# Kernel optimization log

Hardware: AMD Instinct MI355X
Metric: run time of the kernel (lower is better)

Reference implementation:

```python
import jax, jax.numpy as jnp
import numpy as np

CH = 16
HID = 128
UPDATE_RATE = 0.25

def _perception_kernel():
    identity = jnp.array([[0.,0.,0.],[0.,1.,0.],[0.,0.,0.]], jnp.float32)
    sobel_x = jnp.array([[-1.,0.,1.],[-2.,0.,2.],[-1.,0.,1.]], jnp.float32)
    sobel_y = sobel_x.T
    laplacian = jnp.array([[1.,1.,1.],[1.,-8.,1.],[1.,1.,1.]], jnp.float32)
    k = jnp.stack([identity, sobel_x, sobel_y, laplacian])[:, None, :, :]  # [4,1,3,3]
    return jnp.tile(k, (CH, 1, 1, 1))  # [4*CH,1,3,3], OIHW depthwise

def setup_inputs() -> dict:
    key = jax.random.key(0)
    ks = jax.random.split(key, 10)
    B, H, W = 32, 256, 256
    x = jax.random.normal(ks[0], (B, CH, H, W), jnp.float32)
    # 1x1 conv weights: stored as [out,in]; biases [out]
    def lin(k, o, i, scale):
        return jax.random.normal(k, (o, i), jnp.float32) * scale
    w1 = lin(ks[1], HID, CH*4, 1.0/np.sqrt(CH*4)); b1 = jnp.zeros((HID,), jnp.float32)
    w2 = lin(ks[2], HID, HID, 1.0/np.sqrt(HID)); b2 = jnp.zeros((HID,), jnp.float32)
    w3 = lin(ks[3], HID, HID, 1.0/np.sqrt(HID)); b3 = jnp.zeros((HID,), jnp.float32)
    # last layer initialized to zero in original; use small random so gradients flow meaningfully
    w4 = lin(ks[4], CH, HID, 0.01)
    # precomputed random update mask (torch.rand < rate), constant w.r.t. grads
    update_mask = (jax.random.uniform(ks[5], (B, 1, H, W)) < UPDATE_RATE).astype(jnp.float32)
    return {"x": x, "w1": w1, "b1": b1, "w2": w2, "b2": b2, "w3": w3, "b3": b3, "w4": w4, "update_mask": update_mask, "steps": 1}

def _alive_mask(x, threshold=0.01):
    alpha = x[:, :2, :, :]
    pool = jax.lax.reduce_window(alpha, -jnp.inf, jax.lax.max,
                                 (1, 1, 3, 3), (1, 1, 1, 1),
                                 ((0, 0), (0, 0), (1, 1), (1, 1)))
    s = jnp.sum(jnp.abs(pool), axis=1, keepdims=True)  # [B,1,H,W]
    return (s > threshold).astype(x.dtype)

def _step(x, params, update_mask, kernel):
    w1, b1, w2, b2, w3, b3, w4 = params
    pre_alive = _alive_mask(x)
    # depthwise 3x3 perception conv: [B,CH,H,W] -> [B,4*CH,H,W]
    y = jax.lax.conv_general_dilated(x, kernel, (1, 1), ((1, 1), (1, 1)),
                                     dimension_numbers=('NCHW', 'OIHW', 'NCHW'),
                                     feature_group_count=CH)
    lrelu = lambda z: jax.nn.leaky_relu(z, 0.01)
    h = lrelu(jnp.einsum('oc,bchw->bohw', w1, y) + b1[None, :, None, None])
    h = lrelu(jnp.einsum('oc,bchw->bohw', w2, h) + b2[None, :, None, None])
    h = lrelu(jnp.einsum('oc,bchw->bohw', w3, h) + b3[None, :, None, None])
    dy = jnp.einsum('oc,bchw->bohw', w4, h)
    x = x + dy * update_mask
    post_alive = _alive_mask(x)
    return x * (pre_alive * post_alive)

def reference(x, w1, b1, w2, b2, w3, b3, w4, update_mask, steps):
    kernel = _perception_kernel()
    params = (w1, b1, w2, b2, w3, b3, w4)
    for _ in range(steps):
        x = _step(x, params, update_mask, kernel)
    return x
```

## Files before the change

### kernel.cpp

```cpp
#include <hip/hip_runtime.h>

typedef _Float16 f16;
typedef f16 f16x2 __attribute__((ext_vector_type(2)));
typedef f16 f16x8 __attribute__((ext_vector_type(8)));
typedef __fp16 h2v __attribute__((ext_vector_type(2)));
typedef float f32x4 __attribute__((ext_vector_type(4)));
typedef float f32x16 __attribute__((ext_vector_type(16)));
typedef unsigned int uint;
typedef unsigned short ushort;
typedef unsigned long long ull;

#define NCH 16
#define NB 32
#define NH 256
#define NW 256
#define HW 65536
#define CHW 1048576

#define BIAS_BYTE 90112
#define WS_BYTES 91648
#define LIST_OFF WS_BYTES
#define CTR_OFF (WS_BYTES + 12*256*2)
#define LDS_TOTAL (CTR_OFF + 16)

__global__ void prep_k(const float* __restrict__ w1, const float* __restrict__ w2,
                       const float* __restrict__ w3, const float* __restrict__ w4,
                       const float* __restrict__ b1, const float* __restrict__ b2,
                       const float* __restrict__ b3, float* __restrict__ wsf) {
  f16* wf = (f16*)wsf;
  int id = blockIdx.x * 256 + threadIdx.x;
  if (id < 8192) {
    int j = id & 7, l = (id >> 3) & 63, mt = (id >> 9) & 3, kt = id >> 11;
    int o = mt * 32 + (l & 31), c = kt * 16 + (l >> 5) * 8 + j;
    wf[id] = (f16)w1[o * 64 + c];
  } else if (id < 24576) {
    int t = id - 8192;
    int j = t & 7, l = (t >> 3) & 63, mt = (t >> 9) & 3, kt = t >> 11;
    int o = mt * 32 + (l & 31), c = kt * 16 + (l >> 5) * 8 + j;
    wf[8192 + t] = (f16)w2[o * 128 + c];
  } else if (id < 40960) {
    int t = id - 24576;
    int j = t & 7, l = (t >> 3) & 63, mt = (t >> 9) & 3, kt = t >> 11;
    int o = mt * 32 + (l & 31), c = kt * 16 + (l >> 5) * 8 + j;
    wf[24576 + t] = (f16)w3[o * 128 + c];
  } else if (id < 45056) {
    int t = id - 40960;
    int j = t & 7, l = (t >> 3) & 63, kt = t >> 9;
    int m = l & 31, hh = l >> 5;
    int c = kt * 16 + hh * 8 + j;
    wf[40960 + t] = (m < 16) ? (f16)w4[m * 128 + c] : (f16)0.f;
  } else if (id < 45440) {
    int t = id - 45056;
    int r = t & 15, hh = (t >> 4) & 1, mt = (t >> 5) & 3, ly = t >> 7;
    const float* bb = (ly == 0) ? b1 : (ly == 1) ? b2 : b3;
    ((float*)((unsigned char*)wsf + BIAS_BYTE))[t] =
        bb[mt * 32 + (r & 3) + 8 * (r >> 2) + 4 * hh];
  }
}

__global__ __launch_bounds__(256)
void copy_k(const float4* __restrict__ x4, float4* __restrict__ xn4) {
  const size_t total = (size_t)NB * CHW / 4;
  for (size_t i = (size_t)blockIdx.x * 256 + threadIdx.x; i < total; i += (size_t)2048 * 256)
    xn4[i] = x4[i];
}

__device__ __forceinline__ void pl32swap(uint& a, uint& b) {
  asm volatile("v_permlane32_swap_b32 %0, %1" : "+v"(a), "+v"(b));
}

__device__ __forceinline__ f16x8 mk8(uint a, uint b, uint c, uint d) {
  union { uint u[4]; f16x8 v; } z;
  z.u[0] = a; z.u[1] = b; z.u[2] = c; z.u[3] = d;
  return z.v;
}

template <int NKT>
__device__ __forceinline__ void gemm_half(const unsigned char* __restrict__ smem,
                                          int wfFragBase, int biasFloatOff, int lane, int hi,
                                          const f16x8* __restrict__ B, f32x16 acc[4]) {
#pragma unroll
  for (int mt = 0; mt < 4; ++mt) {
    const f32x16* bp =
        (const f32x16*)(smem + BIAS_BYTE + 4 * (biasFloatOff + (mt * 2 + hi) * 16));
    acc[mt] = *bp;
  }
  const f16x8* A = (const f16x8*)smem + wfFragBase + lane;
  __builtin_amdgcn_s_setprio(1);
#pragma unroll
  for (int kt = 0; kt < NKT; ++kt) {
#pragma unroll
    for (int mt = 0; mt < 4; ++mt) {
      f16x8 a = A[(kt * 4 + mt) * 64];
      acc[mt] = __builtin_amdgcn_mfma_f32_32x32x16_f16(a, B[kt], acc[mt], 0, 0, 0);
    }
  }
  __builtin_amdgcn_s_setprio(0);
}

__device__ __forceinline__ void epilogue_swap(const f32x16 acc[4], f16x8 Bn[8]) {
  uint w[32];
  const h2v c001 = {(__fp16)0.01f, (__fp16)0.01f};
#pragma unroll
  for (int mt = 0; mt < 4; ++mt) {
#pragma unroll
    for (int i = 0; i < 8; ++i) {
      h2v u = __builtin_amdgcn_cvt_pkrtz(acc[mt][2 * i], acc[mt][2 * i + 1]);
      h2v s = u * c001;
      h2v m = __builtin_elementwise_max(u, s);
      w[mt * 8 + i] = __builtin_bit_cast(uint, m);
    }
  }
#pragma unroll
  for (int kt = 0; kt < 8; ++kt) {
    int mt = kt >> 1, sub = kt & 1;
    int W = mt * 8 + sub * 4;
    uint a0 = w[W], a1 = w[W + 1], a2 = w[W + 2], a3 = w[W + 3];
    pl32swap(a0, a2);
    pl32swap(a1, a3);
    Bn[kt] = mk8(a0, a1, a2, a3);
  }
}

__device__ __forceinline__ void perc_gpx(const float* __restrict__ xb, int row, int col,
                                         int hi, f16x8 B1h[4]) {
  const bool fU = row > 0, fD = row < NH - 1, fL = col > 0, fR = col < NW - 1;
  const int rU = fU ? row - 1 : row, rD = fD ? row + 1 : row;
  const int cL = fL ? col - 1 : col, cR = fR ? col + 1 : col;
  uint yw[16];
#pragma unroll
  for (int kt = 0; kt < 4; ++kt) {
#pragma unroll
    for (int cp = 0; cp < 2; ++cp) {
      const int c = kt * 4 + hi * 2 + cp;
      const float* base = xb + ((size_t)c << 16);
      const float* pm = base + (row << 8);
      const float* pu = base + (rU << 8);
      const float* pd = base + (rD << 8);
      float v11 = pm[col];
      float v10 = fL ? pm[cL] : 0.f;
      float v12 = fR ? pm[cR] : 0.f;
      float v01 = fU ? pu[col] : 0.f;
      float v00 = (fU && fL) ? pu[cL] : 0.f;
      float v02 = (fU && fR) ? pu[cR] : 0.f;
      float v21 = fD ? pd[col] : 0.f;
      float v20 = (fD && fL) ? pd[cL] : 0.f;
      float v22 = (fD && fR) ? pd[cR] : 0.f;
      float rs0 = v00 + v01 + v02, rs2 = v20 + v21 + v22;
      float fsx = (v02 - v00) + (v22 - v20) + 2.f * (v12 - v10);
      float fsy = (rs2 - rs0) + (v21 - v01);
      float flap = (rs0 + rs2 + v10 + v12) - 8.f * v11;
      h2v t0 = __builtin_amdgcn_cvt_pkrtz(v11, fsx);
      h2v t1 = __builtin_amdgcn_cvt_pkrtz(fsy, flap);
      yw[kt * 4 + cp * 2 + 0] = __builtin_bit_cast(uint, t0);
      yw[kt * 4 + cp * 2 + 1] = __builtin_bit_cast(uint, t1);
    }
  }
#pragma unroll
  for (int kt = 0; kt < 4; ++kt)
    B1h[kt] = mk8(yw[kt * 4], yw[kt * 4 + 1], yw[kt * 4 + 2], yw[kt * 4 + 3]);
}

__global__ __launch_bounds__(768, 1)
void nca_sparse_k(const float* __restrict__ x, const float* __restrict__ wsf,
                  const float* __restrict__ mask, float* __restrict__ xn) {
  extern __shared__ unsigned char smem[];
  ushort* lists = (ushort*)(smem + LIST_OFF);
  int* ctr = (int*)(smem + CTR_OFF);

  const int tid = threadIdx.x;
  const int lane = tid & 63;
  const int wv = tid >> 6;
  const int hi = lane >> 5;

  const int b = blockIdx.x >> 3;
  const int row0 = (blockIdx.x & 7) * 32;
  const float* xb = x + (size_t)b * CHW;
  float* xnb = xn + (size_t)b * CHW;
  const float* mb = mask + (size_t)b * HW;

  {
    const uint4* src = (const uint4*)wsf;
    uint4* dst = (uint4*)smem;
    for (int i = tid; i < WS_BYTES / 16; i += 768) dst[i] = src[i];
  }
  if (tid == 0) *ctr = 0;
  __syncthreads();

  ushort* mylist = lists + wv * 256;

  for (;;) {
    int s;
    if (lane == 0) s = atomicAdd(ctr, 1);
    s = __shfl(s, 0);
    if (s >= 32) break;
    const int row = row0 + s;

    int c = 0;
#pragma unroll
    for (int k2 = 0; k2 < 4; ++k2) {
      int cc = k2 * 64 + lane;
      bool a = mb[(row << 8) + cc] > 0.f;
      ull bal = __ballot(a);
      int rank = __popcll(bal & ((1ull << lane) - 1));
      if (a) mylist[c + rank] = (ushort)cc;
      c += __popcll(bal);
    }
    const int nb = (c + 31) >> 5;

    for (int k = 0; k < nb; ++k) {
      int idx = k * 32 + (lane & 31);
      if (idx >= c) idx = c - 1;
      const int col = mylist[idx];

      f16x8 B1[4];
      perc_gpx(xb, row, col, hi, B1);

      f32x16 acc[4];
      f16x8 B2[8], B3[8], B4[8];
      gemm_half<4>(smem, 0, 0, lane, hi, B1, acc);
      epilogue_swap(acc, B2);
      gemm_half<8>(smem, 1024, 128, lane, hi, B2, acc);
      epilogue_swap(acc, B3);
      gemm_half<8>(smem, 3072, 256, lane, hi, B3, acc);
      epilogue_swap(acc, B4);

      f32x16 a4;
#pragma unroll
      for (int r = 0; r < 16; ++r) a4[r] = 0.f;
      {
        const f16x8* A4 = (const f16x8*)smem + 5120 + lane;
        __builtin_amdgcn_s_setprio(1);
#pragma unroll
        for (int kt = 0; kt < 8; ++kt)
          a4 = __builtin_amdgcn_mfma_f32_32x32x16_f16(A4[kt * 64], B4[kt], a4, 0, 0, 0);
        __builtin_amdgcn_s_setprio(0);
      }

      {
        const float* xrb = xb + (row << 8) + col;
        float* xob = xnb + (row << 8) + col;
#pragma unroll
        for (int r = 0; r < 8; ++r) {
          int ch = (r & 3) + 8 * (r >> 2) + 4 * hi;
          xob[(size_t)ch << 16] = xrb[(size_t)ch << 16] + a4[r];
        }
      }
    }
  }
}

__global__ void alive_scale_k(const float* __restrict__ x, float* __restrict__ xn) {
  __shared__ float pm[4][258];
  const int col = threadIdx.x;
  const int row = blockIdx.x;
  const int b = blockIdx.y;
  const float NEG = -3.0e38f;
  float v0 = NEG, v1 = NEG, v2 = NEG, v3 = NEG;
  const size_t base0 = (size_t)b * CHW + ((size_t)row << 8) + col;
#pragma unroll
  for (int dr = -1; dr <= 1; ++dr) {
    int rr = row + dr;
    if ((unsigned)rr < NH) {
      long o = (long)base0 + dr * NW;
      v0 = fmaxf(v0, x[o]);
      v1 = fmaxf(v1, x[o + HW]);
      v2 = fmaxf(v2, xn[o]);
      v3 = fmaxf(v3, xn[o + HW]);
    }
  }
  pm[0][col + 1] = v0;
  pm[1][col + 1] = v1;
  pm[2][col + 1] = v2;
  pm[3][col + 1] = v3;
  if (col == 0) {
#pragma unroll
    for (int f = 0; f < 4; ++f) { pm[f][0] = NEG; pm[f][257] = NEG; }
  }
  __syncthreads();
  float p0 = fmaxf(fmaxf(pm[0][col], pm[0][col + 1]), pm[0][col + 2]);
  float p1 = fmaxf(fmaxf(pm[1][col], pm[1][col + 1]), pm[1][col + 2]);
  float p2 = fmaxf(fmaxf(pm[2][col], pm[2][col + 1]), pm[2][col + 2]);
  float p3 = fmaxf(fmaxf(pm[3][col], pm[3][col + 1]), pm[3][col + 2]);
  bool alive = ((fabsf(p0) + fabsf(p1)) > 0.01f) && ((fabsf(p2) + fabsf(p3)) > 0.01f);
  if (!alive) {
#pragma unroll
    for (int ch = 0; ch < NCH; ++ch) xn[base0 + ((size_t)ch << 16)] = 0.f;
  }
}

extern "C" void kernel_launch(void* const* d_in, const int* in_sizes, int n_in,
                              void* d_out, int out_size, void* d_ws, size_t ws_size,
                              hipStream_t stream) {
  const float* x    = (const float*)d_in[0];
  const float* w1   = (const float*)d_in[1];
  const float* b1   = (const float*)d_in[2];
  const float* w2   = (const float*)d_in[3];
  const float* b2   = (const float*)d_in[4];
  const float* w3   = (const float*)d_in[5];
  const float* b3   = (const float*)d_in[6];
  const float* w4   = (const float*)d_in[7];
  const float* mask = (const float*)d_in[8];

  float* wsf = (float*)d_ws;
  float* xn = (float*)d_out;

  hipFuncSetAttribute(reinterpret_cast<const void*>(nca_sparse_k),
                      hipFuncAttributeMaxDynamicSharedMemorySize, LDS_TOTAL);

  prep_k<<<178, 256, 0, stream>>>(w1, w2, w3, w4, b1, b2, b3, wsf);
  copy_k<<<2048, 256, 0, stream>>>((const float4*)x, (float4*)xn);
  nca_sparse_k<<<256, 768, LDS_TOTAL, stream>>>(x, wsf, mask, xn);
  alive_scale_k<<<dim3(NH, NB), 256, 0, stream>>>(x, xn);
}
```

Before: 224.2 us.

## Stage x row bands in LDS as fp16 and pool active pixels per band

The sparse NCA kernel now processes 5-row bands per block. Before any compute, it stages 7 rows of all 16 channels into LDS as swizzled fp16, so the 3x3 perception reads come from LDS instead of scattered global gathers. Active pixels from the whole band go into one shared list that all 12 waves pull batches from, which balances load across rows. The costs are extra block-wide barriers per band, converting x to fp16 before the stencil (a small precision change), and a cooperative staging load that also fetches rows where few pixels are active.

```diff
diff --git a/kernel.cpp b/kernel.cpp
--- a/kernel.cpp
+++ b/kernel.cpp
@@ -19,9 +19,16 @@
 
 #define BIAS_BYTE 90112
 #define WS_BYTES 91648
-#define LIST_OFF WS_BYTES
-#define CTR_OFF (WS_BYTES + 12*256*2)
+#define BAND_ROWS 5
+#define STAGE_ROWS 7
+#define XBAND_OFF WS_BYTES
+#define XBAND_BYTES (STAGE_ROWS*256*32)
+#define LIST_OFF (XBAND_OFF + XBAND_BYTES)
+#define LIST_MAX (BAND_ROWS*256)
+#define CTR_OFF (LIST_OFF + LIST_MAX*2)
 #define LDS_TOTAL (CTR_OFF + 16)
+#define NBANDS_PER_IMG 52
+#define NBANDS_TOTAL (NB*NBANDS_PER_IMG)
 
 __global__ void prep_k(const float* __restrict__ w1, const float* __restrict__ w2,
                        const float* __restrict__ w3, const float* __restrict__ w4,
@@ -122,39 +129,39 @@
   }
 }
 
-__device__ __forceinline__ void perc_gpx(const float* __restrict__ xb, int row, int col,
-                                         int hi, f16x8 B1h[4]) {
-  const bool fU = row > 0, fD = row < NH - 1, fL = col > 0, fR = col < NW - 1;
-  const int rU = fU ? row - 1 : row, rD = fD ? row + 1 : row;
-  const int cL = fL ? col - 1 : col, cR = fR ? col + 1 : col;
+__device__ __forceinline__ void perc_band(const unsigned char* __restrict__ xband,
+                                          int rl, int c, int hi, f16x8 B1h[4]) {
+  const bool fL = c > 0, fR = c < NW - 1;
+  const int cm = fL ? c - 1 : c, cp2 = fR ? c + 1 : c;
+  const int swm = (hi ^ (cm & 1)) << 4;
+  const int swc = (hi ^ (c & 1)) << 4;
+  const int swp = (hi ^ (cp2 & 1)) << 4;
+  union U4 { uint4 u; f16 hh[8]; };
+  U4 q[9];
+#pragma unroll
+  for (int dr = 0; dr < 3; ++dr) {
+    const unsigned char* rowp = xband + (size_t)(rl + dr) * 256 * 32;
+    q[dr * 3 + 0].u = *(const uint4*)(rowp + cm * 32 + swm);
+    q[dr * 3 + 1].u = *(const uint4*)(rowp + c * 32 + swc);
+    q[dr * 3 + 2].u = *(const uint4*)(rowp + cp2 * 32 + swp);
+  }
   uint yw[16];
 #pragma unroll
-  for (int kt = 0; kt < 4; ++kt) {
-#pragma unroll
-    for (int cp = 0; cp < 2; ++cp) {
-      const int c = kt * 4 + hi * 2 + cp;
-      const float* base = xb + ((size_t)c << 16);
-      const float* pm = base + (row << 8);
-      const float* pu = base + (rU << 8);
-      const float* pd = base + (rD << 8);
-      float v11 = pm[col];
-      float v10 = fL ? pm[cL] : 0.f;
-      float v12 = fR ? pm[cR] : 0.f;
-      float v01 = fU ? pu[col] : 0.f;
-      float v00 = (fU && fL) ? pu[cL] : 0.f;
-      float v02 = (fU && fR) ? pu[cR] : 0.f;
-      float v21 = fD ? pd[col] : 0.f;
-      float v20 = (fD && fL) ? pd[cL] : 0.f;
-      float v22 = (fD && fR) ? pd[cR] : 0.f;
-      float rs0 = v00 + v01 + v02, rs2 = v20 + v21 + v22;
-      float fsx = (v02 - v00) + (v22 - v20) + 2.f * (v12 - v10);
-      float fsy = (rs2 - rs0) + (v21 - v01);
-      float flap = (rs0 + rs2 + v10 + v12) - 8.f * v11;
-      h2v t0 = __builtin_amdgcn_cvt_pkrtz(v11, fsx);
-      h2v t1 = __builtin_amdgcn_cvt_pkrtz(fsy, flap);
-      yw[kt * 4 + cp * 2 + 0] = __builtin_bit_cast(uint, t0);
-      yw[kt * 4 + cp * 2 + 1] = __builtin_bit_cast(uint, t1);
-    }
+  for (int j = 0; j < 8; ++j) {
+    float v00 = (float)q[0].hh[j], v01 = (float)q[1].hh[j], v02 = (float)q[2].hh[j];
+    float v10 = (float)q[3].hh[j], v11 = (float)q[4].hh[j], v12 = (float)q[5].hh[j];
+    float v20 = (float)q[6].hh[j], v21 = (float)q[7].hh[j], v22 = (float)q[8].hh[j];
+    if (!fL) { v00 = 0.f; v10 = 0.f; v20 = 0.f; }
+    if (!fR) { v02 = 0.f; v12 = 0.f; v22 = 0.f; }
+    float rs0 = v00 + v01 + v02, rs2 = v20 + v21 + v22;
+    float fsx = (v02 - v00) + (v22 - v20) + 2.f * (v12 - v10);
+    float fsy = (rs2 - rs0) + (v21 - v01);
+    float flap = (rs0 + rs2 + v10 + v12) - 8.f * v11;
+    h2v t0 = __builtin_amdgcn_cvt_pkrtz(v11, fsx);
+    h2v t1 = __builtin_amdgcn_cvt_pkrtz(fsy, flap);
+    int kt = j >> 1, cp = j & 1;
+    yw[kt * 4 + cp * 2 + 0] = __builtin_bit_cast(uint, t0);
+    yw[kt * 4 + cp * 2 + 1] = __builtin_bit_cast(uint, t1);
   }
 #pragma unroll
   for (int kt = 0; kt < 4; ++kt)
@@ -162,10 +169,11 @@
 }
 
 __global__ __launch_bounds__(768, 1)
-void nca_sparse_k(const float* __restrict__ x, const float* __restrict__ wsf,
-                  const float* __restrict__ mask, float* __restrict__ xn) {
+void nca_band_k(const float* __restrict__ x, const float* __restrict__ wsf,
+                const float* __restrict__ mask, float* __restrict__ xn) {
   extern __shared__ unsigned char smem[];
-  ushort* lists = (ushort*)(smem + LIST_OFF);
+  unsigned char* xband = smem + XBAND_OFF;
+  ushort* list = (ushort*)(smem + LIST_OFF);
   int* ctr = (int*)(smem + CTR_OFF);
 
   const int tid = threadIdx.x;
@@ -173,48 +181,76 @@
   const int wv = tid >> 6;
   const int hi = lane >> 5;
 
-  const int b = blockIdx.x >> 3;
-  const int row0 = (blockIdx.x & 7) * 32;
-  const float* xb = x + (size_t)b * CHW;
-  float* xnb = xn + (size_t)b * CHW;
-  const float* mb = mask + (size_t)b * HW;
-
   {
     const uint4* src = (const uint4*)wsf;
     uint4* dst = (uint4*)smem;
     for (int i = tid; i < WS_BYTES / 16; i += 768) dst[i] = src[i];
   }
-  if (tid == 0) *ctr = 0;
   __syncthreads();
 
-  ushort* mylist = lists + wv * 256;
-
-  for (;;) {
-    int s;
-    if (lane == 0) s = atomicAdd(ctr, 1);
-    s = __shfl(s, 0);
-    if (s >= 32) break;
-    const int row = row0 + s;
-
-    int c = 0;
-#pragma unroll
-    for (int k2 = 0; k2 < 4; ++k2) {
-      int cc = k2 * 64 + lane;
-      bool a = mb[(row << 8) + cc] > 0.f;
-      ull bal = __ballot(a);
-      int rank = __popcll(bal & ((1ull << lane) - 1));
-      if (a) mylist[c + rank] = (ushort)cc;
-      c += __popcll(bal);
-    }
-    const int nb = (c + 31) >> 5;
-
-    for (int k = 0; k < nb; ++k) {
+  for (int band = blockIdx.x; band < NBANDS_TOTAL; band += 256) {
+    const int b = band / NBANDS_PER_IMG;
+    const int r0 = (band - b * NBANDS_PER_IMG) * BAND_ROWS;
+    const float* xb = x + (size_t)b * CHW;
+    float* xnb = xn + (size_t)b * CHW;
+    const float* mb = mask + (size_t)b * HW;
+
+    if (tid == 0) *ctr = 0;
+    __syncthreads();
+
+    for (int e = tid; e < STAGE_ROWS * 16 * 64; e += 768) {
+      int cg = e & 63;
+      int pair = e >> 6;
+      int sr = pair >> 4;
+      int ch = pair & 15;
+      int gr = r0 - 1 + sr;
+      f32x4 v = {0.f, 0.f, 0.f, 0.f};
+      if ((unsigned)gr < (unsigned)NH)
+        v = *(const f32x4*)(xb + ((size_t)ch << 16) + (gr << 8) + cg * 4);
+      int half = (ch >> 1) & 1;
+      int j = (ch >> 2) * 2 + (ch & 1);
+      unsigned char* base = xband + (size_t)(sr * 256 + cg * 4) * 32;
+#pragma unroll
+      for (int k = 0; k < 4; ++k) {
+        *(f16*)(base + k * 32 + ((half ^ (k & 1)) << 4) + j * 2) = (f16)v[k];
+      }
+    }
+
+    if (wv < BAND_ROWS) {
+      int row = r0 + wv;
+      if (row < NH) {
+        ull bal[4];
+        int c = 0;
+#pragma unroll
+        for (int k = 0; k < 4; ++k) {
+          bool a = mb[(row << 8) + k * 64 + lane] > 0.f;
+          bal[k] = __ballot(a);
+          c += __popcll(bal[k]);
+        }
+        int base;
+        if (lane == 0) base = atomicAdd(ctr, c);
+        base = __shfl(base, 0);
+#pragma unroll
+        for (int k = 0; k < 4; ++k) {
+          int rank = __popcll(bal[k] & ((1ull << lane) - 1));
+          if ((bal[k] >> lane) & 1ull)
+            list[base + rank] = (ushort)((wv << 8) | (k * 64 + lane));
+          base += __popcll(bal[k]);
+        }
+      }
+    }
+    __syncthreads();
+
+    const int n = *ctr;
+    const int nbatch = (n + 31) >> 5;
+    for (int k = wv; k < nbatch; k += 12) {
       int idx = k * 32 + (lane & 31);
-      if (idx >= c) idx = c - 1;
-      const int col = mylist[idx];
+      if (idx >= n) idx = n - 1;
+      const int entry = list[idx];
+      const int rl = entry >> 8, c = entry & 255;
 
       f16x8 B1[4];
-      perc_gpx(xb, row, col, hi, B1);
+      perc_band(xband, rl, c, hi, B1);
 
       f32x16 acc[4];
       f16x8 B2[8], B3[8], B4[8];
@@ -238,8 +274,9 @@
       }
 
       {
-        const float* xrb = xb + (row << 8) + col;
-        float* xob = xnb + (row << 8) + col;
+        const int row = r0 + rl;
+        const float* xrb = xb + (row << 8) + c;
+        float* xob = xnb + (row << 8) + c;
 #pragma unroll
         for (int r = 0; r < 8; ++r) {
           int ch = (r & 3) + 8 * (r >> 2) + 4 * hi;
@@ -247,6 +284,7 @@
         }
       }
     }
+    __syncthreads();
   }
 }
 
@@ -305,11 +343,11 @@
   float* wsf = (float*)d_ws;
   float* xn = (float*)d_out;
 
-  hipFuncSetAttribute(reinterpret_cast<const void*>(nca_sparse_k),
+  hipFuncSetAttribute(reinterpret_cast<const void*>(nca_band_k),
                       hipFuncAttributeMaxDynamicSharedMemorySize, LDS_TOTAL);
 
   prep_k<<<178, 256, 0, stream>>>(w1, w2, w3, w4, b1, b2, b3, wsf);
   copy_k<<<2048, 256, 0, stream>>>((const float4*)x, (float4*)xn);
-  nca_sparse_k<<<256, 768, LDS_TOTAL, stream>>>(x, wsf, mask, xn);
+  nca_band_k<<<256, 768, LDS_TOTAL, stream>>>(x, wsf, mask, xn);
   alive_scale_k<<<dim3(NH, NB), 256, 0, stream>>>(x, xn);
 }
```

Result: faster. 218.4 us (-2.6%).
